# Performance work log

Measured on AMD Instinct MI355X. Metric: run time of the kernel, lower is better.

Reference implementation:

```python
import jax, jax.numpy as jnp
import numpy as np

NUM_NODES = 100000
NUM_RELS = 500
DIM = 64          # input_dim == hidden_dim == output_dim
NUM_EDGES = 1_000_000
LEAKY_SLOPE = 0.01  # torch F.leaky_relu default


def _linear_params(key, fin, fout):
    # torch nn.Linear default init: U(-1/sqrt(fin), 1/sqrt(fin))
    kw, kb = jax.random.split(key)
    s = 1.0 / np.sqrt(fin)
    W = jax.random.uniform(kw, (fout, fin), minval=-s, maxval=s, dtype=jnp.float32)
    b = jax.random.uniform(kb, (fout,), minval=-s, maxval=s, dtype=jnp.float32)
    return W, b


def setup_inputs() -> dict:
    key = jax.random.key(0)
    ks = jax.random.split(key, 12)
    src_idx = jax.random.randint(ks[0], (NUM_EDGES,), 0, NUM_NODES, dtype=jnp.int32)
    dst_idx = jax.random.randint(ks[1], (NUM_EDGES,), 0, NUM_NODES, dtype=jnp.int32)
    rel_idx = jax.random.randint(ks[2], (NUM_EDGES,), 0, NUM_RELS, dtype=jnp.int32)
    ent_embed = jax.random.normal(ks[3], (NUM_NODES, DIM), dtype=jnp.float32)
    rel_embed = jax.random.normal(ks[4], (NUM_RELS, DIM), dtype=jnp.float32)
    W_ent, b_ent = _linear_params(ks[5], DIM, DIM)          # fc_ent
    W_relL, b_relL = _linear_params(ks[6], DIM, DIM)        # fc_rel
    W_rel2, b_rel2 = _linear_params(ks[7], DIM, DIM)        # fc_rel2
    W_rel3, b_rel3 = _linear_params(ks[8], 3 * DIM, DIM)    # fc_rel3
    W_a, b_a = _linear_params(ks[9], DIM, 1)                # a
    W_fc, b_fc = _linear_params(ks[10], 3 * DIM, DIM)       # fc
    return {
        "ent_embed": ent_embed, "rel_embed": rel_embed,
        "W_ent": W_ent, "b_ent": b_ent,
        "W_relL": W_relL, "b_relL": b_relL,
        "W_rel2": W_rel2, "b_rel2": b_rel2,
        "W_rel3": W_rel3, "b_rel3": b_rel3,
        "W_a": W_a, "b_a": b_a,
        "W_fc": W_fc, "b_fc": b_fc,
        "src_idx": src_idx, "dst_idx": dst_idx, "rel_idx": rel_idx,
    }


def reference(ent_embed, rel_embed, W_ent, b_ent, W_relL, b_relL,
              W_rel2, b_rel2, W_rel3, b_rel3, W_a, b_a, W_fc, b_fc,
              src_idx, dst_idx, rel_idx):
    # --- per-edge projections (first=True path: lookup from learned tables) ---
    src = ent_embed[src_idx] @ W_ent.T + b_ent            # [E, D]
    dst = ent_embed[dst_idx] @ W_ent.T + b_ent            # [E, D]
    rel = rel_embed[rel_idx] @ W_relL.T + b_relL          # [E, D]

    # --- edge message c and unnormalized attention b ---
    c = jnp.concatenate([src, dst, rel], axis=1) @ W_fc.T + b_fc   # [E, D]
    logits = jax.nn.leaky_relu((c @ W_a.T + b_a)[:, 0], LEAKY_SLOPE)  # [E]
    b = jnp.exp(logits)                                    # [E] (original uses plain exp)

    # --- scatter-softmax over edges grouped by source node ---
    b_sum = jax.ops.segment_sum(b, src_idx, num_segments=NUM_NODES)  # [N]
    alpha = b / b_sum[src_idx]                             # [E]

    # --- attention-weighted neighbor aggregation ---
    h_ent = jax.ops.segment_sum(alpha[:, None] * c, src_idx,
                                num_segments=NUM_NODES)    # [N, D]

    # --- relation pooling: mean over edges of each relation ---
    rel2 = rel @ W_rel2.T + b_rel2                         # [E, D]
    feats = jnp.concatenate([h_ent[src_idx], h_ent[dst_idx], rel2], axis=1)  # [E, 3D]
    sums = jax.ops.segment_sum(feats, rel_idx, num_segments=NUM_RELS)        # [R, 3D]
    counts = jax.ops.segment_sum(jnp.ones_like(b), rel_idx, num_segments=NUM_RELS)
    mean = sums / jnp.maximum(counts, 1.0)[:, None]        # [R, 3D]

    h_rel = mean @ W_rel3.T + b_rel3                       # [R, D]
    return (h_ent, h_rel)
```

## Files before the change

kernel.cpp:

```cpp
#include <hip/hip_runtime.h>
#include <hip/hip_fp16.h>
#include <math.h>

#define N_NODES 100000
#define N_RELS  500
#define DIM     64
#define N_EDGES 1000000
#define SLOPE   0.01f
#define RSUB    4
#define SC_EDGES 2048
#define NB_E    489
#define NBKT    196
#define BSH     9
#define NROWS   (N_RELS + NBKT)
#define BMAX    5632

__device__ __forceinline__ unsigned short f2bf(float f) {
    unsigned int u = __float_as_uint(f);
    u += 0x7FFFu + ((u >> 16) & 1u);
    return (unsigned short)(u >> 16);
}
__device__ __forceinline__ float bfl(unsigned int u) { return __uint_as_float(u << 16); }
__device__ __forceinline__ float bfh(unsigned int u) { return __uint_as_float(u & 0xFFFF0000u); }

__device__ __forceinline__ unsigned int f2e5m2(float f) {
    __half h = __float2half_rn(f);
    unsigned short hu;
    __builtin_memcpy(&hu, &h, 2);
    unsigned int u = hu;
    u += 0x7Fu + ((u >> 8) & 1u);
    return (u >> 8) & 0xFFu;
}
__device__ __forceinline__ float e5d(unsigned int b) {
    unsigned short u = (unsigned short)(b << 8);
    __half h;
    __builtin_memcpy(&h, &u, 2);
    return __half2float(h);
}
__device__ __forceinline__ void acc8(float* a, unsigned int x, unsigned int y) {
    a[0] += e5d(x & 255u);         a[1] += e5d((x >> 8) & 255u);
    a[2] += e5d((x >> 16) & 255u); a[3] += e5d(x >> 24);
    a[4] += e5d(y & 255u);         a[5] += e5d((y >> 8) & 255u);
    a[6] += e5d((y >> 16) & 255u); a[7] += e5d(y >> 24);
}
__device__ __forceinline__ void acc16(float* a, uint4 w) {
    acc8(a, w.x, w.y);
    acc8(a + 8, w.z, w.w);
}

__global__ void k_fold(const float* __restrict__ W_ent, const float* __restrict__ b_ent,
                       const float* __restrict__ W_relL, const float* __restrict__ b_relL,
                       const float* __restrict__ W_rel2, const float* __restrict__ b_rel2,
                       const float* __restrict__ W_fc, const float* __restrict__ b_fc,
                       float* __restrict__ Wcat, float* __restrict__ dcat,
                       float* __restrict__ MW, float* __restrict__ MQ,
                       float* __restrict__ dW, float* __restrict__ dQ) {
    int idx = blockIdx.x * 256 + threadIdx.x;
    if (idx < 8192) {
        int k = idx >> 7;
        int j2 = idx & 127;
        int jj = j2 & 63;
        int off = (j2 >> 6) * 64;
        float s = 0.f;
        for (int i = 0; i < 64; i++) s += W_fc[jj*192 + off + i] * W_ent[i*64 + k];
        Wcat[k*128 + j2] = s;
    } else if (idx < 12288) {
        int rem = idx - 8192;
        int j = rem >> 6, i = rem & 63;
        float s = 0.f;
        for (int k = 0; k < 64; k++) s += W_fc[j*192 + 128 + k] * W_relL[k*64 + i];
        MW[j*64 + i] = s;
    } else if (idx < 16384) {
        int rem = idx - 12288;
        int j = rem >> 6, i = rem & 63;
        float s = 0.f;
        for (int k = 0; k < 64; k++) s += W_rel2[j*64 + k] * W_relL[k*64 + i];
        MQ[j*64 + i] = s;
    } else if (idx < 16512) {
        int j2 = idx - 16384;
        int jj = j2 & 63;
        int off = (j2 >> 6) * 64;
        float s = 0.f;
        for (int i = 0; i < 64; i++) s += b_ent[i] * W_fc[jj*192 + off + i];
        dcat[j2] = s;
    } else if (idx < 16640) {
        int rem = idx - 16512;
        int vec = rem >> 6, j = rem & 63;
        if (vec == 0) {
            float s = b_fc[j];
            for (int k = 0; k < 64; k++) s += b_relL[k] * W_fc[j*192 + 128 + k];
            dW[j] = s;
        } else {
            float s = b_rel2[j];
            for (int k = 0; k < 64; k++) s += b_relL[k] * W_rel2[j*64 + k];
            dQ[j] = s;
        }
    }
}

__global__ __launch_bounds__(256) void k_node(const float* __restrict__ ent,
        const float* __restrict__ Wcat, const float* __restrict__ dcat,
        const float* __restrict__ W_a,
        float* __restrict__ Uout, unsigned short* __restrict__ V16,
        float* __restrict__ us, float* __restrict__ vs) {
    __shared__ float sA[64][68];
    __shared__ float sW[64][128];
    int t = threadIdx.x;
    int tile0 = blockIdx.x * 64;
    for (int i = t; i < 2048; i += 256)
        ((float4*)sW)[i] = ((const float4*)Wcat)[i];
    for (int f = t; f < 1024; f += 256) {
        int n = f >> 4, k4 = f & 15;
        float4 v4 = (tile0 + n < N_NODES)
            ? ((const float4*)(ent + (size_t)(tile0 + n) * 64))[k4]
            : make_float4(0.f, 0.f, 0.f, 0.f);
        *(float4*)&sA[n][k4 * 4] = v4;
    }
    __syncthreads();

    int ng = t >> 4;
    int jg = t & 15;
    int n0 = ng * 4;
    int j0 = jg * 8;

    float4 d0 = *(const float4*)(dcat + j0);
    float4 d1 = *(const float4*)(dcat + j0 + 4);
    float acc[4][8];
    #pragma unroll
    for (int a = 0; a < 4; a++) {
        acc[a][0] = d0.x; acc[a][1] = d0.y; acc[a][2] = d0.z; acc[a][3] = d0.w;
        acc[a][4] = d1.x; acc[a][5] = d1.y; acc[a][6] = d1.z; acc[a][7] = d1.w;
    }

    #pragma unroll 4
    for (int k = 0; k < 64; k++) {
        float4 w0 = *(const float4*)&sW[k][j0];
        float4 w1 = *(const float4*)&sW[k][j0 + 4];
        float e0 = sA[n0][k], e1 = sA[n0+1][k], e2 = sA[n0+2][k], e3 = sA[n0+3][k];
        float e[4] = {e0, e1, e2, e3};
        #pragma unroll
        for (int a = 0; a < 4; a++) {
            acc[a][0] += e[a] * w0.x; acc[a][1] += e[a] * w0.y;
            acc[a][2] += e[a] * w0.z; acc[a][3] += e[a] * w0.w;
            acc[a][4] += e[a] * w1.x; acc[a][5] += e[a] * w1.y;
            acc[a][6] += e[a] * w1.z; acc[a][7] += e[a] * w1.w;
        }
    }

    int jw = j0 & 63;
    float4 wa0 = *(const float4*)(W_a + jw);
    float4 wa1 = *(const float4*)(W_a + jw + 4);
    float part[4];
    #pragma unroll
    for (int a = 0; a < 4; a++) {
        part[a] = acc[a][0]*wa0.x + acc[a][1]*wa0.y + acc[a][2]*wa0.z + acc[a][3]*wa0.w
                + acc[a][4]*wa1.x + acc[a][5]*wa1.y + acc[a][6]*wa1.z + acc[a][7]*wa1.w;
    }
    #pragma unroll
    for (int m = 1; m <= 4; m <<= 1) {
        #pragma unroll
        for (int a = 0; a < 4; a++) part[a] += __shfl_xor(part[a], m, 64);
    }
    if ((jg & 7) == 0) {
        float* sv = (jg < 8) ? us : vs;
        #pragma unroll
        for (int a = 0; a < 4; a++)
            if (tile0 + n0 + a < N_NODES) sv[tile0 + n0 + a] = part[a];
    }

    #pragma unroll
    for (int a = 0; a < 4; a++) {
        int n = tile0 + n0 + a;
        if (n >= N_NODES) break;
        if (jg < 8) {
            float4 o0 = make_float4(acc[a][0], acc[a][1], acc[a][2], acc[a][3]);
            float4 o1 = make_float4(acc[a][4], acc[a][5], acc[a][6], acc[a][7]);
            float* base = Uout + (size_t)n * 64 + j0;
            *(float4*)(base) = o0;
            *(float4*)(base + 4) = o1;
        } else {
            uint4 pv;
            pv.x = (unsigned int)f2bf(acc[a][0]) | ((unsigned int)f2bf(acc[a][1]) << 16);
            pv.y = (unsigned int)f2bf(acc[a][2]) | ((unsigned int)f2bf(acc[a][3]) << 16);
            pv.z = (unsigned int)f2bf(acc[a][4]) | ((unsigned int)f2bf(acc[a][5]) << 16);
            pv.w = (unsigned int)f2bf(acc[a][6]) | ((unsigned int)f2bf(acc[a][7]) << 16);
            *(uint4*)(V16 + (size_t)n * 64 + (j0 - 64)) = pv;
        }
    }
}

__global__ __launch_bounds__(256, 2) void k_relproj(const float* __restrict__ relE,
        const float* __restrict__ MW, const float* __restrict__ MQ,
        const float* __restrict__ dW, const float* __restrict__ dQ,
        const float* __restrict__ W_a,
        unsigned short* __restrict__ Wr16, float* __restrict__ Qr, float* __restrict__ wsr) {
    int lane = threadIdx.x & 63;
    int wv = threadIdx.x >> 6;
    float mw[64], mq[64];
    #pragma unroll
    for (int i = 0; i < 64; i++) { mw[i] = MW[lane*64 + i]; mq[i] = MQ[lane*64 + i]; }
    float dw = dW[lane], dq = dQ[lane], wa = W_a[lane];
    int r = blockIdx.x * 4 + wv;
    if (r >= N_RELS) return;
    float e = relE[(size_t)r * 64 + lane];
    float w = dw, q = dq;
    #pragma unroll
    for (int i = 0; i < 64; i++) {
        float ei = __shfl(e, i, 64);
        w += ei * mw[i];
        q += ei * mq[i];
    }
    Wr16[(size_t)r * 64 + lane] = f2bf(w);
    Qr[(size_t)r * 64 + lane] = q;
    float tw = w * wa;
    #pragma unroll
    for (int o = 32; o; o >>= 1) tw += __shfl_xor(tw, o, 64);
    if (lane == 0) wsr[r] = tw;
}

__global__ void k_zero(int* __restrict__ a, int n) {
    int g = blockIdx.x * 256 + threadIdx.x;
    if (g < n) a[g] = 0;
}

__global__ __launch_bounds__(256) void k_hist(const int* __restrict__ src, const int* __restrict__ rel,
        int* __restrict__ cnt_rel, int* __restrict__ bucket_cnt, int* __restrict__ blkhist) {
    __shared__ int lcntR[N_RELS];
    __shared__ int lcntS[NBKT];
    int t = threadIdx.x;
    for (int r = t; r < N_RELS; r += 256) lcntR[r] = 0;
    for (int b = t; b < NBKT; b += 256) lcntS[b] = 0;
    __syncthreads();
    int base = blockIdx.x * SC_EDGES;
    if (base + SC_EDGES <= N_EDGES) {
        int e0 = base + t * 8;
        int4 sa = *(const int4*)(src + e0);
        int4 sb = *(const int4*)(src + e0 + 4);
        int4 ra = *(const int4*)(rel + e0);
        int4 rb = *(const int4*)(rel + e0 + 4);
        atomicAdd(&lcntS[sa.x >> BSH], 1); atomicAdd(&lcntS[sa.y >> BSH], 1);
        atomicAdd(&lcntS[sa.z >> BSH], 1); atomicAdd(&lcntS[sa.w >> BSH], 1);
        atomicAdd(&lcntS[sb.x >> BSH], 1); atomicAdd(&lcntS[sb.y >> BSH], 1);
        atomicAdd(&lcntS[sb.z >> BSH], 1); atomicAdd(&lcntS[sb.w >> BSH], 1);
        atomicAdd(&lcntR[ra.x], 1); atomicAdd(&lcntR[ra.y], 1);
        atomicAdd(&lcntR[ra.z], 1); atomicAdd(&lcntR[ra.w], 1);
        atomicAdd(&lcntR[rb.x], 1); atomicAdd(&lcntR[rb.y], 1);
        atomicAdd(&lcntR[rb.z], 1); atomicAdd(&lcntR[rb.w], 1);
    } else {
        for (int g = base + t; g < N_EDGES; g += 256) {
            atomicAdd(&lcntS[src[g] >> BSH], 1);
            atomicAdd(&lcntR[rel[g]], 1);
        }
    }
    __syncthreads();
    for (int r = t; r < N_RELS; r += 256) {
        int c = lcntR[r];
        blkhist[(size_t)r * NB_E + blockIdx.x] = c;
        if (c) atomicAdd(&cnt_rel[r], c);
    }
    for (int b = t; b < NBKT; b += 256) {
        int c = lcntS[b];
        blkhist[(size_t)(N_RELS + b) * NB_E + blockIdx.x] = c;
        if (c) atomicAdd(&bucket_cnt[b], c);
    }
}

__global__ void k_scan_two(const int* __restrict__ cnt_rel, const int* __restrict__ bucket_cnt,
                           int* __restrict__ starts) {
    __shared__ int tot[256];
    int t = threadIdx.x;
    const int* cnt = blockIdx.x ? bucket_cnt : cnt_rel;
    int n = blockIdx.x ? NBKT : N_RELS;
    int* out = starts + (blockIdx.x ? N_RELS : 0);
    int myv[4];
    int mySum = 0;
    for (int q = 0; q < 4; q++) {
        int g = t * 4 + q;
        int v = (g < n) ? cnt[g] : 0;
        myv[q] = v; mySum += v;
    }
    tot[t] = mySum;
    __syncthreads();
    for (int o = 1; o < 256; o <<= 1) {
        int u = (t >= o) ? tot[t - o] : 0;
        __syncthreads();
        tot[t] += u;
        __syncthreads();
    }
    int run = tot[t] - mySum;
    for (int q = 0; q < 4; q++) {
        int g = t * 4 + q;
        if (g < n) out[g] = run;
        run += myv[q];
    }
}

__global__ __launch_bounds__(256) void k_scan_relblk(const int* __restrict__ starts,
        const int* __restrict__ blkhist, int* __restrict__ blkbase) {
    int lane = threadIdx.x & 63;
    int row = (blockIdx.x * 256 + threadIdx.x) >> 6;
    if (row >= NROWS) return;
    int run = starts[row];
    for (int base = 0; base < NB_E; base += 64) {
        int b = base + lane;
        int v = (b < NB_E) ? blkhist[(size_t)row * NB_E + b] : 0;
        int x = v;
        #pragma unroll
        for (int o = 1; o < 64; o <<= 1) {
            int y = __shfl_up(x, o, 64);
            if (lane >= o) x += y;
        }
        if (b < NB_E) blkbase[(size_t)row * NB_E + b] = run + (x - v);
        run += __shfl(x, 63, 64);
    }
}

__global__ __launch_bounds__(256) void k_scatter(const int* __restrict__ src, const int* __restrict__ dst,
        const int* __restrict__ rel, const int* __restrict__ blkbase,
        int2* __restrict__ pay_rel, int* __restrict__ stg_a, int* __restrict__ stg_b) {
    __shared__ int lbaseR[N_RELS];
    __shared__ int loffR[N_RELS];
    __shared__ int lbaseS[NBKT];
    __shared__ int loffS[NBKT];
    int t = threadIdx.x;
    for (int r = t; r < N_RELS; r += 256) {
        lbaseR[r] = blkbase[(size_t)r * NB_E + blockIdx.x];
        loffR[r] = 0;
    }
    for (int b = t; b < NBKT; b += 256) {
        lbaseS[b] = blkbase[(size_t)(N_RELS + b) * NB_E + blockIdx.x];
        loffS[b] = 0;
    }
    __syncthreads();
    int base = blockIdx.x * SC_EDGES;
    if (base + SC_EDGES <= N_EDGES) {
        int e0 = base + t * 8;
        int4 sa = *(const int4*)(src + e0);
        int4 sb = *(const int4*)(src + e0 + 4);
        int4 da = *(const int4*)(dst + e0);
        int4 db = *(const int4*)(dst + e0 + 4);
        int4 ra = *(const int4*)(rel + e0);
        int4 rb = *(const int4*)(rel + e0 + 4);
        int s[8] = {sa.x, sa.y, sa.z, sa.w, sb.x, sb.y, sb.z, sb.w};
        int d[8] = {da.x, da.y, da.z, da.w, db.x, db.y, db.z, db.w};
        int r8[8] = {ra.x, ra.y, ra.z, ra.w, rb.x, rb.y, rb.z, rb.w};
        int p[8], q[8];
        #pragma unroll
        for (int j = 0; j < 8; j++) q[j] = lbaseR[r8[j]] + atomicAdd(&loffR[r8[j]], 1);
        #pragma unroll
        for (int j = 0; j < 8; j++) p[j] = lbaseS[s[j] >> BSH] + atomicAdd(&loffS[s[j] >> BSH], 1);
        #pragma unroll
        for (int j = 0; j < 8; j++) pay_rel[q[j]] = make_int2(s[j], d[j]);
        #pragma unroll
        for (int j = 0; j < 8; j++) stg_a[p[j]] = d[j];
        #pragma unroll
        for (int j = 0; j < 8; j++) stg_b[p[j]] = ((s[j] & 511) << 9) | r8[j];
    } else {
        for (int g = base + t; g < N_EDGES; g += 256) {
            int s = src[g], d = dst[g], r = rel[g];
            int q = lbaseR[r] + atomicAdd(&loffR[r], 1);
            pay_rel[q] = make_int2(s, d);
            int sb2 = s >> BSH;
            int p = lbaseS[sb2] + atomicAdd(&loffS[sb2], 1);
            stg_a[p] = d;
            stg_b[p] = ((s & 511) << 9) | r;
        }
    }
}

__global__ __launch_bounds__(256) void k_sortb(const int* __restrict__ stg_a,
        const int* __restrict__ stg_b, const int* __restrict__ starts,
        const int* __restrict__ bucket_cnt,
        const float* __restrict__ us, const float* __restrict__ vs,
        const float* __restrict__ wsr, const float* __restrict__ b_a_p,
        int2* __restrict__ pay_src, float* __restrict__ pay_b,
        int* __restrict__ start_src, int* __restrict__ cnt_src,
        float* __restrict__ bsum_arr) {
    __shared__ int hist[512];
    __shared__ int lstart[512];
    __shared__ int loff[512];
    __shared__ int tot[256];
    __shared__ float lbsum[512];
    __shared__ int2 lpay[BMAX];
    int bkt = blockIdx.x;
    int base = starts[N_RELS + bkt];
    int n = bucket_cnt[bkt];
    int t = threadIdx.x;
    float ba = b_a_p[0];
    hist[t] = 0; hist[t + 256] = 0;
    lbsum[t] = 0.f; lbsum[t + 256] = 0.f;
    __syncthreads();
    for (int i = t; i < n; i += 256)
        atomicAdd(&hist[stg_b[base + i] >> 9], 1);
    __syncthreads();
    int v0 = hist[t * 2], v1 = hist[t * 2 + 1];
    int mySum = v0 + v1;
    tot[t] = mySum;
    __syncthreads();
    for (int o = 1; o < 256; o <<= 1) {
        int u = (t >= o) ? tot[t - o] : 0;
        __syncthreads();
        tot[t] += u;
        __syncthreads();
    }
    int run = tot[t] - mySum;
    lstart[t * 2] = run;
    lstart[t * 2 + 1] = run + v0;
    loff[t * 2] = 0;
    loff[t * 2 + 1] = 0;
    int node0 = bkt * 512 + t * 2;
    if (node0 < N_NODES) { start_src[node0] = base + run; cnt_src[node0] = v0; }
    if (node0 + 1 < N_NODES) { start_src[node0 + 1] = base + run + v0; cnt_src[node0 + 1] = v1; }
    __syncthreads();
    bool fits = (n <= BMAX);
    for (int i = t; i < n; i += 256) {
        int bb = stg_b[base + i];
        int d = stg_a[base + i];
        int lo = bb >> 9;
        int pos = lstart[lo] + atomicAdd(&loff[lo], 1);
        if (fits) {
            lpay[pos] = make_int2(d, bb);
        } else {
            int r = bb & 511;
            int s = bkt * 512 + lo;
            float t0 = us[s] + vs[d] + wsr[r] + ba;
            t0 = t0 > 0.f ? t0 : SLOPE * t0;
            float b = expf(t0);
            pay_src[base + pos] = make_int2(d, r);
            pay_b[base + pos] = b;
            atomicAdd(&lbsum[lo], b);
        }
    }
    __syncthreads();
    if (fits) {
        for (int i = t; i < n; i += 256) {
            int2 pr = lpay[i];
            int bb = pr.y;
            int lo = bb >> 9;
            int r = bb & 511;
            int s = bkt * 512 + lo;
            float t0 = us[s] + vs[pr.x] + wsr[r] + ba;
            t0 = t0 > 0.f ? t0 : SLOPE * t0;
            float b = expf(t0);
            pay_src[base + i] = make_int2(pr.x, r);
            pay_b[base + i] = b;
            atomicAdd(&lbsum[lo], b);
        }
        __syncthreads();
    }
    if (node0 < N_NODES) bsum_arr[node0] = lbsum[t * 2];
    if (node0 + 1 < N_NODES) bsum_arr[node0 + 1] = lbsum[t * 2 + 1];
}

__global__ __launch_bounds__(256) void k_attn(const int2* __restrict__ pay,
        const float* __restrict__ pay_b,
        const int* __restrict__ start_src, const int* __restrict__ cnt_src,
        const float* __restrict__ bsum_arr,
        const unsigned short* __restrict__ V16, const unsigned short* __restrict__ Wr16,
        float* __restrict__ h, unsigned char* __restrict__ h8) {
    int lane = threadIdx.x & 63;
    int wv = threadIdx.x >> 6;
    int quarter = lane >> 4;
    int lq = lane & 15;
    int slot = lq >> 3;
    int li = lq & 7;
    int n = blockIdx.x * 16 + wv * 4 + quarter;
    if (n >= N_NODES) return;
    int st = start_src[n];
    int cnt = cnt_src[n];
    if (cnt == 0) {
        if (lq < 8) {
            float* hp = h + (size_t)n * 64 + lq * 8;
            *(float4*)hp = make_float4(0.f, 0.f, 0.f, 0.f);
            *(float4*)(hp + 4) = make_float4(0.f, 0.f, 0.f, 0.f);
            *(uint2*)(h8 + (size_t)n * 64 + lq * 8) = make_uint2(0u, 0u);
        }
        return;
    }
    float inv = 1.f / bsum_arr[n];
    float a[8] = {0.f, 0.f, 0.f, 0.f, 0.f, 0.f, 0.f, 0.f};
    for (int e = slot; e < cnt; e += 4) {
        int eB = e + 2;
        bool vB = eB < cnt;
        int eBc = vB ? eB : e;
        float bA = pay_b[st + e];
        float bB = vB ? pay_b[st + eB] : 0.f;
        int2 pA = pay[st + e];
        int2 pB = pay[st + eBc];
        uint4 vvA = *(const uint4*)(V16 + (size_t)pA.x * 64 + li * 8);
        uint4 wwA = *(const uint4*)(Wr16 + (size_t)pA.y * 64 + li * 8);
        uint4 vvB = *(const uint4*)(V16 + (size_t)pB.x * 64 + li * 8);
        uint4 wwB = *(const uint4*)(Wr16 + (size_t)pB.y * 64 + li * 8);
        a[0] += bA * (bfl(vvA.x) + bfl(wwA.x)) + bB * (bfl(vvB.x) + bfl(wwB.x));
        a[1] += bA * (bfh(vvA.x) + bfh(wwA.x)) + bB * (bfh(vvB.x) + bfh(wwB.x));
        a[2] += bA * (bfl(vvA.y) + bfl(wwA.y)) + bB * (bfl(vvB.y) + bfl(wwB.y));
        a[3] += bA * (bfh(vvA.y) + bfh(wwA.y)) + bB * (bfh(vvB.y) + bfh(wwB.y));
        a[4] += bA * (bfl(vvA.z) + bfl(wwA.z)) + bB * (bfl(vvB.z) + bfl(wwB.z));
        a[5] += bA * (bfh(vvA.z) + bfh(wwA.z)) + bB * (bfh(vvB.z) + bfh(wwB.z));
        a[6] += bA * (bfl(vvA.w) + bfl(wwA.w)) + bB * (bfl(vvB.w) + bfl(wwB.w));
        a[7] += bA * (bfh(vvA.w) + bfh(wwA.w)) + bB * (bfh(vvB.w) + bfh(wwB.w));
    }
    #pragma unroll
    for (int d = 0; d < 8; d++) a[d] += __shfl_xor(a[d], 8, 64);
    if (slot == 0) {
        float* hp = h + (size_t)n * 64 + li * 8;
        float o[8];
        #pragma unroll
        for (int d = 0; d < 8; d++) o[d] = hp[d] + a[d] * inv;
        *(float4*)hp = make_float4(o[0], o[1], o[2], o[3]);
        *(float4*)(hp + 4) = make_float4(o[4], o[5], o[6], o[7]);
        uint2 p8;
        p8.x = f2e5m2(o[0]) | (f2e5m2(o[1]) << 8) | (f2e5m2(o[2]) << 16) | (f2e5m2(o[3]) << 24);
        p8.y = f2e5m2(o[4]) | (f2e5m2(o[5]) << 8) | (f2e5m2(o[6]) << 16) | (f2e5m2(o[7]) << 24);
        *(uint2*)(h8 + (size_t)n * 64 + li * 8) = p8;
    }
}

#define RP_STREAMS 6
__global__ __launch_bounds__(256) void k_relpool(const int2* __restrict__ pay,
        const int* __restrict__ start_rel, const int* __restrict__ cnt_rel,
        const unsigned char* __restrict__ h8, float* __restrict__ acc_rel) {
    int r = blockIdx.x / RSUB;
    int sub = blockIdx.x % RSUB;
    int st = start_rel[r];
    int cnt = cnt_rel[r];
    int t = threadIdx.x;
    int li = t & 3;
    int side = (t >> 2) & 1;
    int j = t >> 3;

    int chunk = (cnt + RSUB - 1) / RSUB;
    int k0 = sub * chunk;
    int k1 = min(k0 + chunk, cnt);
    int len = k1 - k0;

    float a[16];
    #pragma unroll
    for (int d = 0; d < 16; d++) a[d] = 0.f;

    if (len > 0) {
        const int2* pp = pay + st + k0;
        int m[RP_STREAMS]; bool v[RP_STREAMS]; int2 p[RP_STREAMS];
        #pragma unroll
        for (int s = 0; s < RP_STREAMS; s++) {
            m[s] = j + s * 32;
            v[s] = m[s] < len;
            p[s] = v[s] ? pp[m[s]] : make_int2(0, 0);
        }
        for (int base = 0; base < len; base += 32 * RP_STREAMS) {
            uint4 hv[RP_STREAMS];
            #pragma unroll
            for (int s = 0; s < RP_STREAMS; s++) {
                int idx = side ? p[s].y : p[s].x;
                hv[s] = *(const uint4*)(h8 + (size_t)idx * 64 + li * 16);
            }
            int mn[RP_STREAMS]; bool vn[RP_STREAMS]; int2 pn[RP_STREAMS];
            #pragma unroll
            for (int s = 0; s < RP_STREAMS; s++) {
                mn[s] = m[s] + 32 * RP_STREAMS;
                vn[s] = mn[s] < len;
                pn[s] = vn[s] ? pp[mn[s]] : make_int2(0, 0);
            }
            #pragma unroll
            for (int s = 0; s < RP_STREAMS; s++) if (v[s]) acc16(a, hv[s]);
            #pragma unroll
            for (int s = 0; s < RP_STREAMS; s++) { m[s] = mn[s]; v[s] = vn[s]; p[s] = pn[s]; }
        }
    }

    #pragma unroll
    for (int d = 0; d < 16; d++) {
        a[d] += __shfl_xor(a[d], 8, 64);
        a[d] += __shfl_xor(a[d], 16, 64);
        a[d] += __shfl_xor(a[d], 32, 64);
    }

    __shared__ float red[4][8][16];
    int wv = t >> 6;
    int lane = t & 63;
    if (lane < 8) {
        #pragma unroll
        for (int d = 0; d < 16; d++) red[wv][lane][d] = a[d];
    }
    __syncthreads();
    if (t < 128) {
        int sl = t >> 4;
        int d = t & 15;
        float s = red[0][sl][d] + red[1][sl][d] + red[2][sl][d] + red[3][sl][d];
        int sd = sl >> 2;
        int li2 = sl & 3;
        atomicAdd(&acc_rel[r * 128 + sd * 64 + li2 * 16 + d], s);
    }
}

__global__ void k_relfin(const float* __restrict__ acc_rel, const int* __restrict__ cnt_rel,
                         const float* __restrict__ Qr, const float* __restrict__ W_rel3,
                         const float* __restrict__ b_rel3, float* __restrict__ out) {
    int g = blockIdx.x * 256 + threadIdx.x;
    if (g >= N_RELS * 64) return;
    int r = g >> 6;
    int j = g & 63;
    int cnt = cnt_rel[r];
    float invc = 1.f / (float)(cnt > 0 ? cnt : 1);
    float s = b_rel3[j];
    for (int k = 0; k < 128; k++) s += acc_rel[r * 128 + k] * invc * W_rel3[j * 192 + k];
    if (cnt > 0)
        for (int k = 0; k < 64; k++) s += Qr[r * 64 + k] * W_rel3[j * 192 + 128 + k];
    out[g] = s;
}

extern "C" void kernel_launch(void* const* d_in, const int* in_sizes, int n_in,
                              void* d_out, int out_size, void* d_ws, size_t ws_size,
                              hipStream_t stream) {
    const float* ent    = (const float*)d_in[0];
    const float* relE   = (const float*)d_in[1];
    const float* W_ent  = (const float*)d_in[2];
    const float* b_ent  = (const float*)d_in[3];
    const float* W_relL = (const float*)d_in[4];
    const float* b_relL = (const float*)d_in[5];
    const float* W_rel2 = (const float*)d_in[6];
    const float* b_rel2 = (const float*)d_in[7];
    const float* W_rel3 = (const float*)d_in[8];
    const float* b_rel3 = (const float*)d_in[9];
    const float* W_a    = (const float*)d_in[10];
    const float* b_a    = (const float*)d_in[11];
    const float* W_fc   = (const float*)d_in[12];
    const float* b_fc   = (const float*)d_in[13];
    const int* src = (const int*)d_in[14];
    const int* dst = (const int*)d_in[15];
    const int* rel = (const int*)d_in[16];
    float* out = (float*)d_out;

    char* ws = (char*)d_ws;
    size_t off = 0;
    auto alloc = [&](size_t bytes) -> void* {
        void* p = ws + off;
        off += (bytes + 255) & ~(size_t)255;
        return p;
    };
    float* Wcat = (float*)alloc(8192 * 4);
    float* dcat = (float*)alloc(128 * 4);
    float* MW  = (float*)alloc(4096 * 4);
    float* MQ  = (float*)alloc(4096 * 4);
    float* dW  = (float*)alloc(64 * 4);
    float* dQ  = (float*)alloc(64 * 4);
    unsigned short* V16 = (unsigned short*)alloc((size_t)N_NODES * 64 * 2);
    unsigned char* h8 = (unsigned char*)alloc((size_t)N_NODES * 64);
    float* us  = (float*)alloc((size_t)N_NODES * 4);
    float* vs  = (float*)alloc((size_t)N_NODES * 4);
    unsigned short* Wr16 = (unsigned short*)alloc((size_t)N_RELS * 64 * 2);
    float* Qr  = (float*)alloc((size_t)N_RELS * 64 * 4);
    float* wsr = (float*)alloc((size_t)N_RELS * 4);
    int* cnt_src   = (int*)alloc((size_t)N_NODES * 4);
    int* start_src = (int*)alloc((size_t)N_NODES * 4);
    float* bsum    = (float*)alloc((size_t)N_NODES * 4);
    int* cnts      = (int*)alloc((size_t)NROWS * 4);
    int* starts    = (int*)alloc((size_t)NROWS * 4);
    int* blkhist   = (int*)alloc((size_t)NROWS * NB_E * 4);
    int* blkbase   = (int*)alloc((size_t)NROWS * NB_E * 4);
    int* stg_a     = (int*)alloc((size_t)N_EDGES * 4);
    int* stg_b     = (int*)alloc((size_t)N_EDGES * 4);
    int2* pay_src  = (int2*)alloc((size_t)N_EDGES * 8);
    float* pay_b   = (float*)alloc((size_t)N_EDGES * 4);
    int2* pay_rel  = (int2*)alloc((size_t)N_EDGES * 8);
    float* acc_rel = (float*)alloc((size_t)N_RELS * 128 * 4);

    int* cnt_rel    = cnts;
    int* bucket_cnt = cnts + N_RELS;

    k_zero<<<(NROWS + 255) / 256, 256, 0, stream>>>(cnts, NROWS);
    k_zero<<<(N_RELS * 128 + 255) / 256, 256, 0, stream>>>((int*)acc_rel, N_RELS * 128);

    k_fold<<<65, 256, 0, stream>>>(W_ent, b_ent, W_relL, b_relL, W_rel2, b_rel2,
                                   W_fc, b_fc, Wcat, dcat, MW, MQ, dW, dQ);
    k_node<<<(N_NODES + 63) / 64, 256, 0, stream>>>(ent, Wcat, dcat, W_a, out, V16, us, vs);
    k_relproj<<<125, 256, 0, stream>>>(relE, MW, MQ, dW, dQ, W_a, Wr16, Qr, wsr);
    k_hist<<<NB_E, 256, 0, stream>>>(src, rel, cnt_rel, bucket_cnt, blkhist);
    k_scan_two<<<2, 256, 0, stream>>>(cnt_rel, bucket_cnt, starts);
    k_scan_relblk<<<(NROWS * 64 + 255) / 256, 256, 0, stream>>>(starts, blkhist, blkbase);
    k_scatter<<<NB_E, 256, 0, stream>>>(src, dst, rel, blkbase, pay_rel, stg_a, stg_b);
    k_sortb<<<NBKT, 256, 0, stream>>>(stg_a, stg_b, starts, bucket_cnt,
                                      us, vs, wsr, b_a,
                                      pay_src, pay_b, start_src, cnt_src, bsum);
    k_attn<<<(N_NODES + 15) / 16, 256, 0, stream>>>(pay_src, pay_b, start_src, cnt_src,
                                                    bsum, V16, Wr16, out, h8);
    k_relpool<<<N_RELS * RSUB, 256, 0, stream>>>(pay_rel, starts, cnt_rel, h8, acc_rel);
    k_relfin<<<(N_RELS * 64 + 255) / 256, 256, 0, stream>>>(acc_rel, cnt_rel, Qr, W_rel3,
                                                            b_rel3, out + (size_t)N_NODES * 64);
}
```

Baseline: 290.9 us.

## Compute softmax denominators in attention kernel and widen bucket sort blocks

The per-source softmax denominator is no longer built with shared-memory float atomics in the bucket-sort kernel. The attention kernel now sums the edge weights it already loads and reduces them with the same shuffle used for the feature accumulators. The sort kernel moves from 256 to 1024 threads per block, so each of the 196 buckets uses more threads to hide latency on its serial passes. The cost is a larger block with idle threads during the scan phase, plus a slightly different floating-point summation order for the denominator.

```diff
diff --git a/kernel.cpp b/kernel.cpp
--- a/kernel.cpp
+++ b/kernel.cpp
@@ -368,52 +368,54 @@
     }
 }
 
-__global__ __launch_bounds__(256) void k_sortb(const int* __restrict__ stg_a,
+__global__ __launch_bounds__(1024) void k_sortb(const int* __restrict__ stg_a,
         const int* __restrict__ stg_b, const int* __restrict__ starts,
         const int* __restrict__ bucket_cnt,
         const float* __restrict__ us, const float* __restrict__ vs,
         const float* __restrict__ wsr, const float* __restrict__ b_a_p,
         int2* __restrict__ pay_src, float* __restrict__ pay_b,
-        int* __restrict__ start_src, int* __restrict__ cnt_src,
-        float* __restrict__ bsum_arr) {
+        int* __restrict__ start_src, int* __restrict__ cnt_src) {
     __shared__ int hist[512];
     __shared__ int lstart[512];
     __shared__ int loff[512];
     __shared__ int tot[256];
-    __shared__ float lbsum[512];
     __shared__ int2 lpay[BMAX];
     int bkt = blockIdx.x;
     int base = starts[N_RELS + bkt];
     int n = bucket_cnt[bkt];
     int t = threadIdx.x;
     float ba = b_a_p[0];
-    hist[t] = 0; hist[t + 256] = 0;
-    lbsum[t] = 0.f; lbsum[t + 256] = 0.f;
-    __syncthreads();
-    for (int i = t; i < n; i += 256)
+    if (t < 512) hist[t] = 0;
+    __syncthreads();
+    for (int i = t; i < n; i += 1024)
         atomicAdd(&hist[stg_b[base + i] >> 9], 1);
     __syncthreads();
-    int v0 = hist[t * 2], v1 = hist[t * 2 + 1];
-    int mySum = v0 + v1;
-    tot[t] = mySum;
+    int v0 = 0, v1 = 0, mySum = 0;
+    if (t < 256) {
+        v0 = hist[t * 2]; v1 = hist[t * 2 + 1];
+        mySum = v0 + v1;
+        tot[t] = mySum;
+    }
     __syncthreads();
     for (int o = 1; o < 256; o <<= 1) {
-        int u = (t >= o) ? tot[t - o] : 0;
+        int u = (t < 256 && t >= o) ? tot[t - o] : 0;
         __syncthreads();
-        tot[t] += u;
+        if (t < 256) tot[t] += u;
         __syncthreads();
     }
-    int run = tot[t] - mySum;
-    lstart[t * 2] = run;
-    lstart[t * 2 + 1] = run + v0;
-    loff[t * 2] = 0;
-    loff[t * 2 + 1] = 0;
-    int node0 = bkt * 512 + t * 2;
-    if (node0 < N_NODES) { start_src[node0] = base + run; cnt_src[node0] = v0; }
-    if (node0 + 1 < N_NODES) { start_src[node0 + 1] = base + run + v0; cnt_src[node0 + 1] = v1; }
+    if (t < 256) {
+        int run = tot[t] - mySum;
+        lstart[t * 2] = run;
+        lstart[t * 2 + 1] = run + v0;
+        loff[t * 2] = 0;
+        loff[t * 2 + 1] = 0;
+        int node0 = bkt * 512 + t * 2;
+        if (node0 < N_NODES) { start_src[node0] = base + run; cnt_src[node0] = v0; }
+        if (node0 + 1 < N_NODES) { start_src[node0 + 1] = base + run + v0; cnt_src[node0 + 1] = v1; }
+    }
     __syncthreads();
     bool fits = (n <= BMAX);
-    for (int i = t; i < n; i += 256) {
+    for (int i = t; i < n; i += 1024) {
         int bb = stg_b[base + i];
         int d = stg_a[base + i];
         int lo = bb >> 9;
@@ -425,15 +427,13 @@
             int s = bkt * 512 + lo;
             float t0 = us[s] + vs[d] + wsr[r] + ba;
             t0 = t0 > 0.f ? t0 : SLOPE * t0;
-            float b = expf(t0);
             pay_src[base + pos] = make_int2(d, r);
-            pay_b[base + pos] = b;
-            atomicAdd(&lbsum[lo], b);
+            pay_b[base + pos] = expf(t0);
         }
     }
     __syncthreads();
     if (fits) {
-        for (int i = t; i < n; i += 256) {
+        for (int i = t; i < n; i += 1024) {
             int2 pr = lpay[i];
             int bb = pr.y;
             int lo = bb >> 9;
@@ -441,21 +441,15 @@
             int s = bkt * 512 + lo;
             float t0 = us[s] + vs[pr.x] + wsr[r] + ba;
             t0 = t0 > 0.f ? t0 : SLOPE * t0;
-            float b = expf(t0);
             pay_src[base + i] = make_int2(pr.x, r);
-            pay_b[base + i] = b;
-            atomicAdd(&lbsum[lo], b);
-        }
-        __syncthreads();
-    }
-    if (node0 < N_NODES) bsum_arr[node0] = lbsum[t * 2];
-    if (node0 + 1 < N_NODES) bsum_arr[node0 + 1] = lbsum[t * 2 + 1];
+            pay_b[base + i] = expf(t0);
+        }
+    }
 }
 
 __global__ __launch_bounds__(256) void k_attn(const int2* __restrict__ pay,
         const float* __restrict__ pay_b,
         const int* __restrict__ start_src, const int* __restrict__ cnt_src,
-        const float* __restrict__ bsum_arr,
         const unsigned short* __restrict__ V16, const unsigned short* __restrict__ Wr16,
         float* __restrict__ h, unsigned char* __restrict__ h8) {
     int lane = threadIdx.x & 63;
@@ -477,8 +471,8 @@
         }
         return;
     }
-    float inv = 1.f / bsum_arr[n];
     float a[8] = {0.f, 0.f, 0.f, 0.f, 0.f, 0.f, 0.f, 0.f};
+    float bs = 0.f;
     for (int e = slot; e < cnt; e += 4) {
         int eB = e + 2;
         bool vB = eB < cnt;
@@ -491,6 +485,7 @@
         uint4 wwA = *(const uint4*)(Wr16 + (size_t)pA.y * 64 + li * 8);
         uint4 vvB = *(const uint4*)(V16 + (size_t)pB.x * 64 + li * 8);
         uint4 wwB = *(const uint4*)(Wr16 + (size_t)pB.y * 64 + li * 8);
+        bs += bA + bB;
         a[0] += bA * (bfl(vvA.x) + bfl(wwA.x)) + bB * (bfl(vvB.x) + bfl(wwB.x));
         a[1] += bA * (bfh(vvA.x) + bfh(wwA.x)) + bB * (bfh(vvB.x) + bfh(wwB.x));
         a[2] += bA * (bfl(vvA.y) + bfl(wwA.y)) + bB * (bfl(vvB.y) + bfl(wwB.y));
@@ -502,7 +497,9 @@
     }
     #pragma unroll
     for (int d = 0; d < 8; d++) a[d] += __shfl_xor(a[d], 8, 64);
+    bs += __shfl_xor(bs, 8, 64);
     if (slot == 0) {
+        float inv = 1.f / bs;
         float* hp = h + (size_t)n * 64 + li * 8;
         float o[8];
         #pragma unroll
@@ -653,7 +650,6 @@
     float* wsr = (float*)alloc((size_t)N_RELS * 4);
     int* cnt_src   = (int*)alloc((size_t)N_NODES * 4);
     int* start_src = (int*)alloc((size_t)N_NODES * 4);
-    float* bsum    = (float*)alloc((size_t)N_NODES * 4);
     int* cnts      = (int*)alloc((size_t)NROWS * 4);
     int* starts    = (int*)alloc((size_t)NROWS * 4);
     int* blkhist   = (int*)alloc((size_t)NROWS * NB_E * 4);
@@ -679,11 +675,11 @@
     k_scan_two<<<2, 256, 0, stream>>>(cnt_rel, bucket_cnt, starts);
     k_scan_relblk<<<(NROWS * 64 + 255) / 256, 256, 0, stream>>>(starts, blkhist, blkbase);
     k_scatter<<<NB_E, 256, 0, stream>>>(src, dst, rel, blkbase, pay_rel, stg_a, stg_b);
-    k_sortb<<<NBKT, 256, 0, stream>>>(stg_a, stg_b, starts, bucket_cnt,
-                                      us, vs, wsr, b_a,
-                                      pay_src, pay_b, start_src, cnt_src, bsum);
+    k_sortb<<<NBKT, 1024, 0, stream>>>(stg_a, stg_b, starts, bucket_cnt,
+                                       us, vs, wsr, b_a,
+                                       pay_src, pay_b, start_src, cnt_src);
     k_attn<<<(N_NODES + 15) / 16, 256, 0, stream>>>(pay_src, pay_b, start_src, cnt_src,
-                                                    bsum, V16, Wr16, out, h8);
+                                                    V16, Wr16, out, h8);
     k_relpool<<<N_RELS * RSUB, 256, 0, stream>>>(pay_rel, starts, cnt_rel, h8, acc_rel);
     k_relfin<<<(N_RELS * 64 + 255) / 256, 256, 0, stream>>>(acc_rel, cnt_rel, Qr, W_rel3,
                                                             b_rel3, out + (size_t)N_NODES * 64);
```

After: 288.7 us. No clear change (-0.8%).
